# Kernel optimization log

Hardware: AMD Instinct MI355X
Metric: run time of the kernel (lower is better)

## Reference

```python
import jax, jax.numpy as jnp
import numpy as np

N = 100000      # total nodes
G = 500         # graphs
NPG = 200       # nodes per graph
E = 1_600_000   # edges
XS = 128        # input feature dim
FIX = 10        # fixed_size one-hot id dim
H = 64          # hidden (neuron)
NPERM = 3
YS = 1


def setup_inputs() -> dict:
    key = jax.random.key(0)
    ks = jax.random.split(key, 10)
    x = jax.random.normal(ks[0], (N, XS), jnp.float32)

    rng = np.random.default_rng(0)
    src = rng.integers(0, N, E)
    off = rng.integers(1, NPG, E)
    dst = (src // NPG) * NPG + (src % NPG + off) % NPG  # edges stay within graph
    edge_index = jnp.asarray(np.stack([src, dst]).astype(np.int32))
    batch_ids = jnp.asarray((np.arange(N) // NPG).astype(np.int32))

    # permuted tiled-eye node ids: node at local pos p gets one_hot(perm[p] % 10)
    base = np.arange(NPG) % FIX  # tiled eye row indices for one graph
    ids = rng.permuted(np.tile(base, (NPERM, G, 1)), axis=-1).reshape(NPERM, N)
    perm_ids = jax.nn.one_hot(jnp.asarray(ids), FIX, dtype=jnp.float32)

    def lin(k, fin, fout):
        return jax.random.normal(k, (fin, fout), jnp.float32) * (1.0 / np.sqrt(fin))

    return {
        "x": x, "edge_index": edge_index, "batch_ids": batch_ids, "perm_ids": perm_ids,
        "w1": lin(ks[1], XS + FIX, H), "b1": jnp.zeros((H,), jnp.float32),
        "w2": lin(ks[2], H, H), "b2": jnp.zeros((H,), jnp.float32),
        "w3": lin(ks[3], H, H), "b3": jnp.zeros((H,), jnp.float32),
        "a1w": lin(ks[4], H, 16), "a1b": jnp.zeros((16,), jnp.float32),
        "a2w": lin(ks[5], 16, YS), "a2b": jnp.zeros((YS,), jnp.float32),
    }


def reference(x, edge_index, batch_ids, perm_ids,
              w1, b1, w2, b2, w3, b3, a1w, a1b, a2w, a2b):
    src, dst = edge_index[0], edge_index[1]
    loop = jnp.arange(N, dtype=src.dtype)
    src_a = jnp.concatenate([src, loop])  # GCNConv adds self-loops
    dst_a = jnp.concatenate([dst, loop])
    deg = jax.ops.segment_sum(jnp.ones_like(dst_a, x.dtype), dst_a, N)
    dinv = jnp.where(deg > 0, deg ** -0.5, 0.0)
    norm = (dinv[src_a] * dinv[dst_a])[:, None]  # [E+N, 1]

    def conv(h, W, b):
        h = h @ W  # transform first (cheaper: H <= in_dim)
        return jax.ops.segment_sum(h[src_a] * norm, dst_a, N) + b

    counts = jnp.maximum(jax.ops.segment_sum(jnp.ones((N,), x.dtype), batch_ids, G), 1.0)

    out = jnp.zeros((G, H), x.dtype)
    for p in range(NPERM):
        h = jnp.concatenate([x, perm_ids[p]], axis=1)  # [N, XS+FIX]
        h = jax.nn.relu(conv(h, w1, b1))
        h = jax.nn.relu(conv(h, w2, b2))
        h = jax.nn.relu(conv(h, w3, b3))
        hg = jax.ops.segment_sum(h, batch_ids, G) / counts[:, None]  # mean pool
        out = out + hg / NPERM

    out = jax.nn.relu(out @ a1w + a1b)
    return out @ a2w + a2b  # [G, YS]
```

## Files before the change

### kernel.cpp

```cpp
#include <hip/hip_runtime.h>

#define NN   100000
#define EE   1600000
#define GG   500
#define NPGc 200
#define NPERMc 3
#define ASTRIDE (208 * 224)

typedef __fp16   h16x2 __attribute__((ext_vector_type(2)));
typedef _Float16 f16x4 __attribute__((ext_vector_type(4)));
typedef _Float16 f16x8 __attribute__((ext_vector_type(8)));
typedef float    f32x4 __attribute__((ext_vector_type(4)));

__device__ __forceinline__ void cvt_hilo(f32x4 a, f32x4 b, f16x8& hi, f16x8& lo) {
    float f[8] = {a[0], a[1], a[2], a[3], b[0], b[1], b[2], b[3]};
#pragma unroll
    for (int j = 0; j < 8; j += 2) {
        h16x2 h = __builtin_amdgcn_cvt_pkrtz(f[j], f[j + 1]);
        h16x2 l = __builtin_amdgcn_cvt_pkrtz(f[j] - (float)h[0], f[j + 1] - (float)h[1]);
        hi[j] = (_Float16)h[0]; hi[j + 1] = (_Float16)h[1];
        lo[j] = (_Float16)l[0]; lo[j + 1] = (_Float16)l[1];
    }
}

__device__ __forceinline__ f16x4 cvt4h(const float (&v)[4]) {
    f16x4 r;
    h16x2 a = __builtin_amdgcn_cvt_pkrtz(v[0], v[1]);
    h16x2 b = __builtin_amdgcn_cvt_pkrtz(v[2], v[3]);
    r[0] = (_Float16)a[0]; r[1] = (_Float16)a[1];
    r[2] = (_Float16)b[0]; r[3] = (_Float16)b[1];
    return r;
}

__device__ __forceinline__ f16x8 wfrag_slot(const float* __restrict__ src, int kstep, int ct,
                                            int term, int mq, int qq) {
    f16x8 v;
#pragma unroll
    for (int j = 0; j < 8; ++j) {
        float wv = src[(kstep * 32 + qq * 8 + j) * 64 + ct * 16 + mq];
        _Float16 hi = (_Float16)wv;
        v[j] = term ? (_Float16)(wv - (float)hi) : hi;
    }
    return v;
}

__device__ __forceinline__ f16x8 cvt_a8(uint2 v) {
    f16x8 r;
#pragma unroll
    for (int k = 0; k < 4; ++k) r[k] = (_Float16)(float)((v.x >> (8 * k)) & 255u);
#pragma unroll
    for (int k = 0; k < 4; ++k) r[4 + k] = (_Float16)(float)((v.y >> (8 * k)) & 255u);
    return r;
}

__global__ __launch_bounds__(256) void k_adj(const int* __restrict__ ei, unsigned int* __restrict__ A) {
    int idx = blockIdx.x * 256 + threadIdx.x;
    if (idx < EE) {
        int s = ei[idx], d = ei[EE + idx];
        int g = s / NPGc;
        int ls = s - g * NPGc, ld = d - g * NPGc;
        int addr = g * ASTRIDE + ld * 224 + ls;
        atomicAdd(&A[addr >> 2], 1u << ((addr & 3) * 8));
    } else if (idx < EE + NN) {
        int n = idx - EE;
        int g = n / NPGc, ln = n - g * NPGc;
        int addr = g * ASTRIDE + ln * 225;
        atomicAdd(&A[addr >> 2], 1u << ((addr & 3) * 8));
    }
}

__global__ __launch_bounds__(512) void k_xw(const float* __restrict__ x,
                                            const float* __restrict__ w1,
                                            float* __restrict__ xW) {
    __shared__ __align__(16) float xs[128 * 132];
    __shared__ __align__(16) _Float16 wf1[32 * 512];

    int t = threadIdx.x;
    int rbase = blockIdx.x * 128;

    for (int i = t; i < 2048; i += 512) {
        int c = i >> 6, lane2 = i & 63;
        ((f16x8*)wf1)[i] = wfrag_slot(w1, c & 3, (c >> 2) & 3, c >> 4, lane2 & 15, lane2 >> 4);
    }
    {
        int row = t >> 5, col4 = t & 31;
#pragma unroll
        for (int pass = 0; pass < 8; ++pass) {
            int r = pass * 16 + row;
            int grow = min(rbase + r, NN - 1);
            *(f32x4*)&xs[r * 132 + col4 * 4] = *(const f32x4*)(x + (size_t)grow * 128 + col4 * 4);
        }
    }
    __syncthreads();

    int lane = t & 63, w = t >> 6;
    int m = lane & 15, q = lane >> 4;
    int rowl = w * 16 + m;
    f16x8 Ah[4], Al[4];
#pragma unroll
    for (int ks = 0; ks < 4; ++ks) {
        f32x4 f0 = *(const f32x4*)&xs[rowl * 132 + ks * 32 + q * 8];
        f32x4 f1 = *(const f32x4*)&xs[rowl * 132 + ks * 32 + q * 8 + 4];
        cvt_hilo(f0, f1, Ah[ks], Al[ks]);
    }
    int rb = rbase + w * 16;
#pragma unroll
    for (int ct = 0; ct < 4; ++ct) {
        f32x4 acc = {0.f, 0.f, 0.f, 0.f};
#pragma unroll
        for (int ks = 0; ks < 4; ++ks) {
            f16x8 Bh = ((const f16x8*)wf1)[((0 * 4 + ct) * 4 + ks) * 64 + lane];
            f16x8 Bl = ((const f16x8*)wf1)[((1 * 4 + ct) * 4 + ks) * 64 + lane];
            acc = __builtin_amdgcn_mfma_f32_16x16x32_f16(Ah[ks], Bh, acc, 0, 0, 0);
            acc = __builtin_amdgcn_mfma_f32_16x16x32_f16(Al[ks], Bh, acc, 0, 0, 0);
            acc = __builtin_amdgcn_mfma_f32_16x16x32_f16(Ah[ks], Bl, acc, 0, 0, 0);
        }
#pragma unroll
        for (int i = 0; i < 4; ++i) {
            int r = rb + q * 4 + i;
            if (r < NN) xW[(size_t)r * 64 + ct * 16 + m] = acc[i];
        }
    }
}

template <bool POOL>
__device__ __forceinline__ void conv_mfma(const _Float16* __restrict__ Tfh,
                                          _Float16* __restrict__ Hf,
                                          const f16x8 (&Af)[2][7], int lane, int m, int q,
                                          int w, int nmt, const float* __restrict__ dv,
                                          const float* __restrict__ biasrow,
                                          float (&poolv)[4]) {
    f32x4 acc[2][4];
#pragma unroll
    for (int mi = 0; mi < 2; ++mi)
#pragma unroll
        for (int ct = 0; ct < 4; ++ct) acc[mi][ct] = (f32x4){0.f, 0.f, 0.f, 0.f};

#pragma unroll
    for (int ks = 0; ks < 7; ++ks) {
#pragma unroll
        for (int ct = 0; ct < 4; ++ct) {
            f16x8 Bh = ((const f16x8*)Tfh)[(ks * 4 + ct) * 64 + lane];
            acc[0][ct] = __builtin_amdgcn_mfma_f32_16x16x32_f16(Af[0][ks], Bh, acc[0][ct], 0, 0, 0);
            if (nmt > 1)
                acc[1][ct] = __builtin_amdgcn_mfma_f32_16x16x32_f16(Af[1][ks], Bh, acc[1][ct], 0, 0, 0);
        }
    }
#pragma unroll
    for (int mi = 0; mi < 2; ++mi) {
        if (mi >= nmt) break;
        int mt = w + 8 * mi;
        int rb = mt * 16 + q * 4;
        float dvi[4];
#pragma unroll
        for (int i = 0; i < 4; ++i) dvi[i] = dv[rb + i];
#pragma unroll
        for (int ct = 0; ct < 4; ++ct) {
            float bias = biasrow[ct * 16 + m];
            if (!POOL) {
#pragma unroll
                for (int i = 0; i < 4; ++i) {
                    float o = fmaxf(fmaf(dvi[i], acc[mi][ct][i], bias), 0.f);
                    Hf[(mt * 2 + (ct >> 1)) * 512 +
                       ((q * 4 + i) + 16 * ((ct & 1) * 2 + (m >> 3))) * 8 + (m & 7)] = (_Float16)o;
                }
            } else {
                float pl = 0.f;
#pragma unroll
                for (int i = 0; i < 4; ++i) {
                    float o = fmaxf(fmaf(dvi[i], acc[mi][ct][i], bias), 0.f);
                    if (rb + i < NPGc) pl += o;
                }
                poolv[ct] += pl;
            }
        }
    }
}

__device__ __forceinline__ void gemm_mfma(const _Float16* __restrict__ Hf,
                                          _Float16* __restrict__ Tfh,
                                          const _Float16* __restrict__ wf, int lane,
                                          int m, int q, int w, int nmt,
                                          const float* __restrict__ dv) {
#pragma unroll
    for (int mi = 0; mi < 2; ++mi) {
        if (mi >= nmt) break;
        int mt = w + 8 * mi;
        f16x8 Ah0 = ((const f16x8*)Hf)[(mt * 2 + 0) * 64 + lane];
        f16x8 Ah1 = ((const f16x8*)Hf)[(mt * 2 + 1) * 64 + lane];
        float dvi[4];
#pragma unroll
        for (int i = 0; i < 4; ++i) dvi[i] = dv[mt * 16 + q * 4 + i];
        int quad = (2 * mt + (q >> 1)) & 3;
        int j0 = (q & 1) << 2;
        int lanep = m + (quad << 4);
#pragma unroll
        for (int ct = 0; ct < 4; ++ct) {
            f32x4 acc = {0.f, 0.f, 0.f, 0.f};
            f16x8 B0 = ((const f16x8*)wf)[(ct * 2 + 0) * 64 + lane];
            f16x8 B1 = ((const f16x8*)wf)[(ct * 2 + 1) * 64 + lane];
            acc = __builtin_amdgcn_mfma_f32_16x16x32_f16(Ah0, B0, acc, 0, 0, 0);
            acc = __builtin_amdgcn_mfma_f32_16x16x32_f16(Ah1, B1, acc, 0, 0, 0);
            float o[4];
#pragma unroll
            for (int i = 0; i < 4; ++i) o[i] = acc[i] * dvi[i];
            *(f16x4*)(Tfh + ((mt >> 1) * 4 + ct) * 512 + lanep * 8 + j0) = cvt4h(o);
        }
    }
}

__global__ __launch_bounds__(512, 4) void k_fused(
    const float* __restrict__ xW, const float* __restrict__ perm,
    const float* __restrict__ w1,
    const float* __restrict__ b1, const float* __restrict__ b2, const float* __restrict__ b3,
    const float* __restrict__ w2, const float* __restrict__ w3,
    const unsigned char* __restrict__ Aall,
    const float* __restrict__ a1w, const float* __restrict__ a1b,
    const float* __restrict__ a2w, const float* __restrict__ a2b,
    float* __restrict__ out) {
    __shared__ __align__(16) _Float16 Tfh[28 * 512];
    __shared__ __align__(16) _Float16 Hf[26 * 512];
    __shared__ __align__(16) _Float16 wlds[16 * 512];
    __shared__ float w1r[640];
    __shared__ float dv[224];
    __shared__ float biasL[192];
    __shared__ float pool[8 * 64];
    __shared__ unsigned char idsl[672];

    int g = blockIdx.x, t = threadIdx.x;
    int lane = t & 63, w = t >> 6;
    int m = lane & 15, q = lane >> 4;
    int nmt = (w < 5) ? 2 : 1;
    int nbase = g * NPGc;

    for (int i = t; i < 1024; i += 512) {
        int c = i >> 6, lane2 = i & 63;
        const float* src = (c >= 8) ? w3 : w2;
        int c4 = c & 7;
        ((f16x8*)wlds)[i] = wfrag_slot(src, c4 & 1, c4 >> 1, 0, lane2 & 15, lane2 >> 4);
    }
    for (int i = t; i < 640; i += 512) w1r[i] = w1[128 * 64 + i];
    if (t < 192) biasL[t] = (t < 64) ? b1[t] : ((t < 128) ? b2[t - 64] : b3[t - 128]);
    for (int i = t; i < 672; i += 512) {
        int p = i / 224, nd = i - p * 224;
        int id = 0;
        if (nd < NPGc) {
            const float* pp = perm + ((size_t)p * NN + nbase + nd) * 10;
            float best = pp[0];
#pragma unroll
            for (int k = 1; k < 10; ++k) { float v = pp[k]; if (v > best) { best = v; id = k; } }
        }
        idsl[i] = (unsigned char)id;
    }
    const unsigned char* Ag = Aall + (size_t)g * ASTRIDE;
    f16x8 Af[2][7];
#pragma unroll
    for (int mi = 0; mi < 2; ++mi) {
        if (mi >= nmt) break;
        int mt = w + 8 * mi;
        unsigned s = 0;
#pragma unroll
        for (int ks = 0; ks < 7; ++ks) {
            uint2 v = *(const uint2*)(Ag + (mt * 16 + m) * 224 + ks * 32 + q * 8);
            Af[mi][ks] = cvt_a8(v);
            s += (v.x & 255u) + ((v.x >> 8) & 255u) + ((v.x >> 16) & 255u) + (v.x >> 24);
            s += (v.y & 255u) + ((v.y >> 8) & 255u) + ((v.y >> 16) & 255u) + (v.y >> 24);
        }
        float tot = (float)s;
        tot += __shfl_xor(tot, 16);
        tot += __shfl_xor(tot, 32);
        if (q == 0) dv[mt * 16 + m] = (tot > 0.f) ? rsqrtf(tot) : 0.f;
    }
    __syncthreads();

    float poolv[4] = {0.f, 0.f, 0.f, 0.f};

    for (int p = 0; p < NPERMc; ++p) {
        {
            const unsigned char* ids = idsl + p * 224;
            for (int nd0 = w * 28; nd0 < w * 28 + 28; nd0 += 4) {
                float vals[4];
#pragma unroll
                for (int i = 0; i < 4; ++i) {
                    int nd = nd0 + i;
                    float v = 0.f;
                    if (nd < NPGc)
                        v = dv[nd] * (xW[(size_t)(nbase + nd) * 64 + lane] + w1r[ids[nd] * 64 + lane]);
                    vals[i] = v;
                }
                int c = (nd0 >> 5) * 4 + (lane >> 4);
                int lanep = (lane & 15) + (((nd0 & 31) >> 3) << 4);
                *(f16x4*)(Tfh + c * 512 + lanep * 8 + (nd0 & 7)) = cvt4h(vals);
            }
        }
        __syncthreads();
        conv_mfma<false>(Tfh, Hf, Af, lane, m, q, w, nmt, dv, biasL, poolv);
        __syncthreads();
        gemm_mfma(Hf, Tfh, wlds, lane, m, q, w, nmt, dv);
        __syncthreads();
        conv_mfma<false>(Tfh, Hf, Af, lane, m, q, w, nmt, dv, biasL + 64, poolv);
        __syncthreads();
        gemm_mfma(Hf, Tfh, wlds + 8 * 512, lane, m, q, w, nmt, dv);
        __syncthreads();
        conv_mfma<true>(Tfh, Hf, Af, lane, m, q, w, nmt, dv, biasL + 128, poolv);
        __syncthreads();
    }

#pragma unroll
    for (int ct = 0; ct < 4; ++ct) {
        float v = poolv[ct];
        v += __shfl_xor(v, 16);
        v += __shfl_xor(v, 32);
        if (q == 0) pool[w * 64 + ct * 16 + m] = v;
    }
    __syncthreads();
    if (t < 64) {
        float tot = 0.f;
#pragma unroll
        for (int i = 0; i < 8; ++i) tot += pool[i * 64 + t];
        pool[t] = tot * (1.0f / (NPGc * NPERMc));
    }
    __syncthreads();
    if (t < 16) {
        float a = a1b[t];
        for (int k = 0; k < 64; ++k) a = fmaf(pool[k], a1w[k * 16 + t], a);
        pool[64 + t] = fmaxf(a, 0.f);
    }
    __syncthreads();
    if (t == 0) {
        float o = a2b[0];
#pragma unroll
        for (int i = 0; i < 16; ++i) o = fmaf(pool[64 + i], a2w[i], o);
        out[g] = o;
    }
}


static inline size_t alignup(size_t x) { return (x + 255) & ~(size_t)255; }

extern "C" void kernel_launch(void* const* d_in, const int* in_sizes, int n_in,
                              void* d_out, int out_size, void* d_ws, size_t ws_size,
                              hipStream_t stream) {
    const float* x    = (const float*)d_in[0];
    const int*   ei   = (const int*)d_in[1];
    const float* perm = (const float*)d_in[3];
    const float* w1   = (const float*)d_in[4];
    const float* b1   = (const float*)d_in[5];
    const float* w2   = (const float*)d_in[6];
    const float* b2   = (const float*)d_in[7];
    const float* w3   = (const float*)d_in[8];
    const float* b3   = (const float*)d_in[9];
    const float* a1w  = (const float*)d_in[10];
    const float* a1b  = (const float*)d_in[11];
    const float* a2w  = (const float*)d_in[12];
    const float* a2b  = (const float*)d_in[13];
    float* out = (float*)d_out;

    char* p = (char*)d_ws;
    auto take = [&](size_t bytes) { char* r = p; p += alignup(bytes); return r; };
    float*         xW   = (float*)take((size_t)NN * 64 * 4);
    unsigned char* Aall = (unsigned char*)take((size_t)GG * ASTRIDE);
    (void)hipMemsetAsync(Aall, 0, (size_t)GG * ASTRIDE, stream);

    k_adj<<<(EE + NN + 255) / 256, 256, 0, stream>>>(ei, (unsigned int*)Aall);
    k_xw<<<(NN + 127) / 128, 512, 0, stream>>>(x, w1, xW);
    k_fused<<<GG, 512, 0, stream>>>(xW, perm, w1, b1, b2, b3, w2, w3, Aall,
                                    a1w, a1b, a2w, a2b, out);
}
```

Before: 319.1 us.

## Bin edges per graph and build dense adjacency in LDS inside fused kernel

```diff
diff --git a/kernel.cpp b/kernel.cpp
--- a/kernel.cpp
+++ b/kernel.cpp
@@ -5,7 +5,9 @@
 #define GG   500
 #define NPGc 200
 #define NPERMc 3
-#define ASTRIDE (208 * 224)
+#define C1   16384
+#define BSTRIDE 4096
+#define EB   98
 
 typedef __fp16   h16x2 __attribute__((ext_vector_type(2)));
 typedef _Float16 f16x4 __attribute__((ext_vector_type(4)));
@@ -53,19 +55,42 @@
     return r;
 }
 
-__global__ __launch_bounds__(256) void k_adj(const int* __restrict__ ei, unsigned int* __restrict__ A) {
-    int idx = blockIdx.x * 256 + threadIdx.x;
-    if (idx < EE) {
-        int s = ei[idx], d = ei[EE + idx];
+__global__ __launch_bounds__(512) void k_bin(const int* __restrict__ ei, int* __restrict__ gcnt,
+                                             unsigned short* __restrict__ gtok) {
+    __shared__ unsigned short stag[C1];
+    __shared__ int h[512], esc[512], cur[512], gb[512];
+    int t = threadIdx.x;
+    int base = blockIdx.x * C1;
+    int nE = min(C1, EE - base);
+    h[t] = 0; cur[t] = 0;
+    __syncthreads();
+    for (int i = t; i < nE; i += 512) atomicAdd(&h[ei[base + i] / NPGc], 1);
+    __syncthreads();
+    esc[t] = h[t];
+    __syncthreads();
+    for (int off = 1; off < 512; off <<= 1) {
+        int u = (t >= off) ? esc[t - off] : 0;
+        __syncthreads();
+        esc[t] += u;
+        __syncthreads();
+    }
+    esc[t] -= h[t];
+    if (t < GG && h[t] > 0) gb[t] = atomicAdd(&gcnt[t], h[t]);
+    __syncthreads();
+    for (int i = t; i < nE; i += 512) {
+        int s = ei[base + i], d = ei[EE + base + i];
         int g = s / NPGc;
         int ls = s - g * NPGc, ld = d - g * NPGc;
-        int addr = g * ASTRIDE + ld * 224 + ls;
-        atomicAdd(&A[addr >> 2], 1u << ((addr & 3) * 8));
-    } else if (idx < EE + NN) {
-        int n = idx - EE;
-        int g = n / NPGc, ln = n - g * NPGc;
-        int addr = g * ASTRIDE + ln * 225;
-        atomicAdd(&A[addr >> 2], 1u << ((addr & 3) * 8));
+        int pos = esc[g] + atomicAdd(&cur[g], 1);
+        stag[pos] = (unsigned short)(ls | (ld << 8));
+    }
+    __syncthreads();
+    int w = t >> 6, lane = t & 63;
+    for (int g = w; g < GG; g += 8) {
+        int c = h[g]; if (!c) continue;
+        int lb = esc[g], off = gb[g];
+        int lim = min(c, BSTRIDE - off);
+        for (int j = lane; j < lim; j += 64) gtok[(size_t)g * BSTRIDE + off + j] = stag[lb + j];
     }
 }
 
@@ -126,7 +151,7 @@
 template <bool POOL>
 __device__ __forceinline__ void conv_mfma(const _Float16* __restrict__ Tfh,
                                           _Float16* __restrict__ Hf,
-                                          const f16x8 (&Af)[2][7], int lane, int m, int q,
+                                          const uint2 (&af)[2][7], int lane, int m, int q,
                                           int w, int nmt, const float* __restrict__ dv,
                                           const float* __restrict__ biasrow,
                                           float (&poolv)[4]) {
@@ -138,12 +163,14 @@
 
 #pragma unroll
     for (int ks = 0; ks < 7; ++ks) {
+        f16x8 A0 = cvt_a8(af[0][ks]);
+        f16x8 A1 = cvt_a8(af[1][ks]);
 #pragma unroll
         for (int ct = 0; ct < 4; ++ct) {
             f16x8 Bh = ((const f16x8*)Tfh)[(ks * 4 + ct) * 64 + lane];
-            acc[0][ct] = __builtin_amdgcn_mfma_f32_16x16x32_f16(Af[0][ks], Bh, acc[0][ct], 0, 0, 0);
+            acc[0][ct] = __builtin_amdgcn_mfma_f32_16x16x32_f16(A0, Bh, acc[0][ct], 0, 0, 0);
             if (nmt > 1)
-                acc[1][ct] = __builtin_amdgcn_mfma_f32_16x16x32_f16(Af[1][ks], Bh, acc[1][ct], 0, 0, 0);
+                acc[1][ct] = __builtin_amdgcn_mfma_f32_16x16x32_f16(A1, Bh, acc[1][ct], 0, 0, 0);
         }
     }
 #pragma unroll
@@ -214,12 +241,11 @@
     const float* __restrict__ w1,
     const float* __restrict__ b1, const float* __restrict__ b2, const float* __restrict__ b3,
     const float* __restrict__ w2, const float* __restrict__ w3,
-    const unsigned char* __restrict__ Aall,
+    const int* __restrict__ gcnt, const unsigned short* __restrict__ gtok,
     const float* __restrict__ a1w, const float* __restrict__ a1b,
     const float* __restrict__ a2w, const float* __restrict__ a2b,
     float* __restrict__ out) {
-    __shared__ __align__(16) _Float16 Tfh[28 * 512];
-    __shared__ __align__(16) _Float16 Hf[26 * 512];
+    __shared__ __align__(16) _Float16 TfHf[54 * 512];
     __shared__ __align__(16) _Float16 wlds[16 * 512];
     __shared__ float w1r[640];
     __shared__ float dv[224];
@@ -227,12 +253,27 @@
     __shared__ float pool[8 * 64];
     __shared__ unsigned char idsl[672];
 
+    _Float16* Tfh = TfHf;
+    _Float16* Hf  = TfHf + 28 * 512;
+    unsigned char* A8  = (unsigned char*)TfHf;
+    unsigned int*  A32 = (unsigned int*)TfHf;
+
     int g = blockIdx.x, t = threadIdx.x;
     int lane = t & 63, w = t >> 6;
     int m = lane & 15, q = lane >> 4;
     int nmt = (w < 5) ? 2 : 1;
     int nbase = g * NPGc;
-
+    int cnt = min(gcnt[g], BSTRIDE);
+    const unsigned short* tok = gtok + (size_t)g * BSTRIDE;
+
+    for (int i = t; i < 2912; i += 512) ((uint4*)A8)[i] = make_uint4(0, 0, 0, 0);
+    __syncthreads();
+    for (int i = t; i < cnt; i += 512) {
+        int tk = tok[i];
+        int addr = (tk >> 8) * 224 + (tk & 255);
+        atomicAdd(&A32[addr >> 2], 1u << ((addr & 3) * 8));
+    }
+    if (t < NPGc) { int a = t * 225; atomicAdd(&A32[a >> 2], 1u << ((a & 3) * 8)); }
     for (int i = t; i < 1024; i += 512) {
         int c = i >> 6, lane2 = i & 63;
         const float* src = (c >= 8) ? w3 : w2;
@@ -252,24 +293,25 @@
         }
         idsl[i] = (unsigned char)id;
     }
-    const unsigned char* Ag = Aall + (size_t)g * ASTRIDE;
-    f16x8 Af[2][7];
+    __syncthreads();
+    if (t < 224) {
+        unsigned s = 0;
+        if (t < 208)
+            for (int i = 0; i < 56; ++i) {
+                unsigned v = A32[t * 56 + i];
+                s += (v & 255u) + ((v >> 8) & 255u) + ((v >> 16) & 255u) + (v >> 24);
+            }
+        dv[t] = s ? rsqrtf((float)s) : 0.f;
+    }
+    uint2 af[2][7];
 #pragma unroll
     for (int mi = 0; mi < 2; ++mi) {
-        if (mi >= nmt) break;
         int mt = w + 8 * mi;
-        unsigned s = 0;
-#pragma unroll
-        for (int ks = 0; ks < 7; ++ks) {
-            uint2 v = *(const uint2*)(Ag + (mt * 16 + m) * 224 + ks * 32 + q * 8);
-            Af[mi][ks] = cvt_a8(v);
-            s += (v.x & 255u) + ((v.x >> 8) & 255u) + ((v.x >> 16) & 255u) + (v.x >> 24);
-            s += (v.y & 255u) + ((v.y >> 8) & 255u) + ((v.y >> 16) & 255u) + (v.y >> 24);
-        }
-        float tot = (float)s;
-        tot += __shfl_xor(tot, 16);
-        tot += __shfl_xor(tot, 32);
-        if (q == 0) dv[mt * 16 + m] = (tot > 0.f) ? rsqrtf(tot) : 0.f;
+#pragma unroll
+        for (int ks = 0; ks < 7; ++ks)
+            af[mi][ks] = (mi < nmt)
+                ? *(const uint2*)(A8 + (mt * 16 + m) * 224 + ks * 32 + q * 8)
+                : make_uint2(0u, 0u);
     }
     __syncthreads();
 
@@ -294,15 +336,15 @@
             }
         }
         __syncthreads();
-        conv_mfma<false>(Tfh, Hf, Af, lane, m, q, w, nmt, dv, biasL, poolv);
+        conv_mfma<false>(Tfh, Hf, af, lane, m, q, w, nmt, dv, biasL, poolv);
         __syncthreads();
         gemm_mfma(Hf, Tfh, wlds, lane, m, q, w, nmt, dv);
         __syncthreads();
-        conv_mfma<false>(Tfh, Hf, Af, lane, m, q, w, nmt, dv, biasL + 64, poolv);
+        conv_mfma<false>(Tfh, Hf, af, lane, m, q, w, nmt, dv, biasL + 64, poolv);
         __syncthreads();
         gemm_mfma(Hf, Tfh, wlds + 8 * 512, lane, m, q, w, nmt, dv);
         __syncthreads();
-        conv_mfma<true>(Tfh, Hf, Af, lane, m, q, w, nmt, dv, biasL + 128, poolv);
+        conv_mfma<true>(Tfh, Hf, af, lane, m, q, w, nmt, dv, biasL + 128, poolv);
         __syncthreads();
     }
 
@@ -358,12 +400,13 @@
 
     char* p = (char*)d_ws;
     auto take = [&](size_t bytes) { char* r = p; p += alignup(bytes); return r; };
-    float*         xW   = (float*)take((size_t)NN * 64 * 4);
-    unsigned char* Aall = (unsigned char*)take((size_t)GG * ASTRIDE);
-    (void)hipMemsetAsync(Aall, 0, (size_t)GG * ASTRIDE, stream);
-
-    k_adj<<<(EE + NN + 255) / 256, 256, 0, stream>>>(ei, (unsigned int*)Aall);
+    float*          xW   = (float*)take((size_t)NN * 64 * 4);
+    unsigned short* gtok = (unsigned short*)take((size_t)GG * BSTRIDE * 2);
+    int*            gcnt = (int*)take(512 * 4);
+    (void)hipMemsetAsync(gcnt, 0, 512 * 4, stream);
+
+    k_bin<<<EB, 512, 0, stream>>>(ei, gcnt, gtok);
     k_xw<<<(NN + 127) / 128, 512, 0, stream>>>(x, w1, xW);
-    k_fused<<<GG, 512, 0, stream>>>(xW, perm, w1, b1, b2, b3, w2, w3, Aall,
-                                    a1w, a1b, a2w, a2b, out);
-}
+    k_fused<<<GG, 512, 0, stream>>>(xW, perm, w1, b1, b2, b3, w2, w3,
+                                    gcnt, gtok, a1w, a1b, a2w, a2b, out);
+}
```

New measurement: 291.4 us. 8.7% less time.
